# Kernel tuning notes

Measured on AMD Instinct MI355X. Metric: run time of the kernel, lower is better.

Reference implementation:

```python
import jax, jax.numpy as jnp
import numpy as np

B, T, S, C, F = 32, 50, 2048, 8, 32  # batch, time, spatial steps, in-channels, filters
K, STRIDE = 2, 2
DN = ('NWC', 'WIO', 'NWC')


def hard_sigmoid(x):
    # TF-Keras hard_sigmoid: clip(0.2*x + 0.5, 0, 1)
    return jnp.clip(0.2 * x + 0.5, 0.0, 1.0)


def setup_inputs() -> dict:
    key = jax.random.key(0)
    ks = jax.random.split(key, 5)
    x = jax.random.normal(ks[0], (B, T, S, C), jnp.float32)
    kernel = jax.random.normal(ks[1], (K, C, 4 * F), jnp.float32) * 0.05
    rec_kernel = jax.random.normal(ks[2], (K, F, 4 * F), jnp.float32) * 0.05
    bias = jnp.zeros((4 * F,), jnp.float32)
    dense_w = jax.random.normal(ks[3], ((S // STRIDE) * F, 1), jnp.float32) * 0.02
    dense_b = jnp.zeros((1,), jnp.float32)
    return dict(x=x, kernel=kernel, rec_kernel=rec_kernel, bias=bias,
                dense_w=dense_w, dense_b=dense_b)


def reference(x, kernel, rec_kernel, bias, dense_w, dense_b):
    b, t, s, c = x.shape
    f = rec_kernel.shape[1]
    # Input convolution for all timesteps at once (stride 2, SAME padding)
    xc = jax.lax.conv_general_dilated(x.reshape(b * t, s, c), kernel,
                                      (STRIDE,), 'SAME', dimension_numbers=DN)
    xc = xc + bias
    sh = xc.shape[1]  # ceil(s / stride)
    xc = xc.reshape(b, t, sh, 4 * f).transpose(1, 0, 2, 3)  # time-major for scan

    def step(carry, xt):
        h, cst = carry
        hc = jax.lax.conv_general_dilated(h, rec_kernel, (1,), 'SAME',
                                          dimension_numbers=DN)
        z = xt + hc
        zi, zf, zc, zo = jnp.split(z, 4, axis=-1)
        i = hard_sigmoid(zi)
        fg = hard_sigmoid(zf)
        cst = fg * cst + i * jnp.tanh(zc)
        o = hard_sigmoid(zo)
        h = o * jnp.tanh(cst)
        return (h, cst), None

    h0 = jnp.zeros((b, sh, f), x.dtype)
    (h, _), _ = jax.lax.scan(step, (h0, h0), xc)
    # Flatten + Dense(1)
    return h.reshape(b, -1) @ dense_w + dense_b
```

## Files before the change

kernel.cpp:

```cpp
#include <hip/hip_runtime.h>


#define TT 50
#define LTILE 64
#define ROWS 129
#define HSTR 40

typedef __attribute__((ext_vector_type(8))) short short8;
typedef __attribute__((ext_vector_type(4))) float floatx4;

__device__ __forceinline__ unsigned short f2b_rne(float f) {
  union { float f; unsigned u; } v; v.f = f;
  unsigned r = v.u + 0x7FFFu + ((v.u >> 16) & 1u);
  return (unsigned short)(r >> 16);
}
__device__ __forceinline__ unsigned short f2b_trunc(float f) {
  union { float f; unsigned u; } v; v.f = f;
  return (unsigned short)(v.u >> 16);
}
__device__ __forceinline__ float hsig(float x) {
  return __builtin_amdgcn_fmed3f(__builtin_fmaf(0.2f, x, 0.5f), 0.0f, 1.0f);
}
__device__ __forceinline__ float ftanh(float x) {
  float e = __expf(2.0f * x);
  return 1.0f - 2.0f * __builtin_amdgcn_rcpf(e + 1.0f);
}

__global__ __launch_bounds__(256, 2)
void convlstm_scan(const float* __restrict__ xs,
                   const float* __restrict__ ks,
                   const float* __restrict__ rks,
                   const float* __restrict__ bs,
                   const float* __restrict__ dws,
                   float* __restrict__ acc_out) {
  __shared__ short hbH[2][ROWS * HSTR];

  const int tid  = threadIdx.x;
  const int b    = blockIdx.x >> 4;
  const int j0   = (blockIdx.x & 15) * LTILE;
  const int wave = tid >> 6;
  const int lane = tid & 63;
  const int q    = lane >> 4;
  const int f0   = lane & 15;

  for (int e = tid; e < ROWS * HSTR; e += 256)
    ((int*)hbH)[e] = 0;

  short8 Bwh0[8], Bwh1[8], Bxw[8];
#pragma unroll
  for (int n = 0; n < 8; ++n) {
    const int oc = (n >> 1) * 32 + 2 * f0 + (n & 1);
    short8 th;
#pragma unroll
    for (int j = 0; j < 8; ++j)
      th[j] = (short)f2b_rne(rks[(q * 8 + j) * 128 + oc]);
    Bwh0[n] = th;
#pragma unroll
    for (int j = 0; j < 8; ++j)
      th[j] = (short)f2b_rne(rks[(32 + q * 8 + j) * 128 + oc]);
    Bwh1[n] = th;
    short8 tx = {0, 0, 0, 0, 0, 0, 0, 0};
    if (q < 2) {
#pragma unroll
      for (int j = 0; j < 8; ++j)
        tx[j] = (short)f2b_rne(ks[(q * 8 + j) * 128 + oc]);
    } else if (q == 2) {
      tx[0] = (short)f2b_rne(bs[oc]);
    }
    Bxw[n] = tx;
  }

  short8 axc = {0, 0, 0, 0, 0, 0, 0, 0};
  if (q == 2) axc[0] = (short)0x3F80;

  const floatx4 zero4 = {0.0f, 0.0f, 0.0f, 0.0f};

  float cst[2][8];
#pragma unroll
  for (int s = 0; s < 2; ++s)
#pragma unroll
    for (int i = 0; i < 8; ++i) cst[s][i] = 0.0f;

  floatx4 px0[2], px1[2];
#pragma unroll
  for (int s = 0; s < 2; ++s) {
    const int jr = (wave + 4 * s) * 16 + f0;
    const int jm = min(j0 + jr, 1023);
    const float* xp = xs + (size_t)b * TT * (2048 * 8) +
                      (size_t)(2 * jm + (q & 1)) * 8;
    px0[s] = *(const floatx4*)xp;
    px1[s] = *(const floatx4*)(xp + 4);
  }

  const int maxrows = 1024 - j0;
  float part = 0.0f;
  __syncthreads();

  for (int t = 0; t < TT; ++t) {
    const short* curH = hbH[t & 1];
    short* nxtH = hbH[(t & 1) ^ 1];
    int rows = LTILE + (TT - 1) - t;
    if (rows > maxrows) rows = maxrows;
    const int nmt = (rows + 15) >> 4;
    const int act1 = (wave + 4) < nmt;
    const int last = (t == TT - 1);
    const int tn = last ? t : t + 1;
    const float* xnext = xs + ((size_t)(b * TT + tn)) * (2048 * 8);

    short8 a0h[2], a1h[2];
#pragma unroll
    for (int s = 0; s < 2; ++s) {
      const int jr = (wave + 4 * s) * 16 + f0;
      a0h[s] = *(const short8*)&curH[jr * HSTR + q * 8];
      a1h[s] = *(const short8*)&curH[(jr + 1) * HSTR + q * 8];
    }

    short8 ax[2];
#pragma unroll
    for (int s = 0; s < 2; ++s) {
      ax[s] = axc;
      if (q < 2) {
        floatx4 x0 = px0[s], x1 = px1[s];
#pragma unroll
        for (int jj = 0; jj < 4; ++jj) ax[s][jj] = (short)f2b_trunc(x0[jj]);
#pragma unroll
        for (int jj = 0; jj < 4; ++jj) ax[s][4 + jj] = (short)f2b_trunc(x1[jj]);
      }
    }

#pragma unroll
    for (int s = 0; s < 2; ++s) {
      const int jr = (wave + 4 * s) * 16 + f0;
      const int jm = min(j0 + jr, 1023);
      const float* xp = xnext + (size_t)(2 * jm + (q & 1)) * 8;
      px0[s] = *(const floatx4*)xp;
      px1[s] = *(const floatx4*)(xp + 4);
    }

#pragma unroll
    for (int s = 0; s < 2; ++s) {
      if (s == 1 && !act1) continue;
      const int m = wave + 4 * s;

      floatx4 acc[8];
#pragma unroll
      for (int n = 0; n < 8; ++n)
        acc[n] = __builtin_amdgcn_mfma_f32_16x16x32_bf16(ax[s], Bxw[n], zero4, 0, 0, 0);
#pragma unroll
      for (int n = 0; n < 8; ++n)
        acc[n] = __builtin_amdgcn_mfma_f32_16x16x32_bf16(a0h[s], Bwh0[n], acc[n], 0, 0, 0);
#pragma unroll
      for (int n = 0; n < 8; ++n)
        acc[n] = __builtin_amdgcn_mfma_f32_16x16x32_bf16(a1h[s], Bwh1[n], acc[n], 0, 0, 0);

      const int jw = m * 16 + q * 4;
#pragma unroll
      for (int r = 0; r < 4; ++r) {
        float hv2[2];
#pragma unroll
        for (int p = 0; p < 2; ++p) {
          float zi = acc[0 + p][r], zf = acc[2 + p][r];
          float zc = acc[4 + p][r], zo = acc[6 + p][r];
          float ig = hsig(zi), fg = hsig(zf), og = hsig(zo);
          float cs = cst[s][p * 4 + r];
          float cn = __builtin_fmaf(fg, cs, ig * ftanh(zc));
          cst[s][p * 4 + r] = cn;
          hv2[p] = og * ftanh(cn);
        }
        if (!last) {
          unsigned pk = (unsigned)f2b_rne(hv2[0]) |
                        ((unsigned)f2b_rne(hv2[1]) << 16);
          *(unsigned*)&nxtH[(jw + r) * HSTR + 2 * f0] = pk;
        } else {
          const int di = (j0 + jw + r) * 32 + 2 * f0;
          part = __builtin_fmaf(hv2[0], dws[di],
                 __builtin_fmaf(hv2[1], dws[di + 1], part));
        }
      }
    }
    __syncthreads();
  }

#pragma unroll
  for (int off = 32; off > 0; off >>= 1) part += __shfl_down(part, off);
  if (lane == 0) atomicAdd(&acc_out[b], part);
}

__global__ void init_acc(float* ws) {
  if (threadIdx.x < 32) ws[threadIdx.x] = 0.0f;
}

__global__ void finalize(const float* __restrict__ ws,
                         const float* __restrict__ db,
                         float* __restrict__ out) {
  int i = threadIdx.x;
  if (i < 32) out[i] = ws[i] + db[0];
}

extern "C" void kernel_launch(void* const* d_in, const int* in_sizes, int n_in,
                              void* d_out, int out_size, void* d_ws, size_t ws_size,
                              hipStream_t stream) {
  const float* x  = (const float*)d_in[0];
  const float* k  = (const float*)d_in[1];
  const float* rk = (const float*)d_in[2];
  const float* bi = (const float*)d_in[3];
  const float* dw = (const float*)d_in[4];
  const float* db = (const float*)d_in[5];
  float* ws = (float*)d_ws;
  float* out = (float*)d_out;

  hipLaunchKernelGGL(init_acc, dim3(1), dim3(64), 0, stream, ws);
  hipLaunchKernelGGL(convlstm_scan, dim3(512), dim3(256), 0, stream,
                     x, k, rk, bi, dw, ws);
  hipLaunchKernelGGL(finalize, dim3(1), dim3(64), 0, stream, ws, db, out);
}
```

Measured before the change: 240.6 us.

## Split gate output columns across two wave halves with 512-thread blocks

```diff
diff --git a/kernel.cpp b/kernel.cpp
--- a/kernel.cpp
+++ b/kernel.cpp
@@ -26,7 +26,7 @@
   return 1.0f - 2.0f * __builtin_amdgcn_rcpf(e + 1.0f);
 }
 
-__global__ __launch_bounds__(256, 2)
+__global__ __launch_bounds__(512, 4)
 void convlstm_scan(const float* __restrict__ xs,
                    const float* __restrict__ ks,
                    const float* __restrict__ rks,
@@ -39,26 +39,28 @@
   const int b    = blockIdx.x >> 4;
   const int j0   = (blockIdx.x & 15) * LTILE;
   const int wave = tid >> 6;
+  const int mw   = wave & 3;
+  const int p    = wave >> 2;
   const int lane = tid & 63;
   const int q    = lane >> 4;
   const int f0   = lane & 15;
 
-  for (int e = tid; e < ROWS * HSTR; e += 256)
+  for (int e = tid; e < ROWS * HSTR; e += 512)
     ((int*)hbH)[e] = 0;
 
-  short8 Bwh0[8], Bwh1[8], Bxw[8];
-#pragma unroll
-  for (int n = 0; n < 8; ++n) {
-    const int oc = (n >> 1) * 32 + 2 * f0 + (n & 1);
+  short8 Bwh0[4], Bwh1[4], Bxw[4];
+#pragma unroll
+  for (int g = 0; g < 4; ++g) {
+    const int oc = g * 32 + 2 * f0 + p;
     short8 th;
 #pragma unroll
     for (int j = 0; j < 8; ++j)
       th[j] = (short)f2b_rne(rks[(q * 8 + j) * 128 + oc]);
-    Bwh0[n] = th;
+    Bwh0[g] = th;
 #pragma unroll
     for (int j = 0; j < 8; ++j)
       th[j] = (short)f2b_rne(rks[(32 + q * 8 + j) * 128 + oc]);
-    Bwh1[n] = th;
+    Bwh1[g] = th;
     short8 tx = {0, 0, 0, 0, 0, 0, 0, 0};
     if (q < 2) {
 #pragma unroll
@@ -67,7 +69,7 @@
     } else if (q == 2) {
       tx[0] = (short)f2b_rne(bs[oc]);
     }
-    Bxw[n] = tx;
+    Bxw[g] = tx;
   }
 
   short8 axc = {0, 0, 0, 0, 0, 0, 0, 0};
@@ -75,16 +77,16 @@
 
   const floatx4 zero4 = {0.0f, 0.0f, 0.0f, 0.0f};
 
-  float cst[2][8];
+  float cst[2][4];
 #pragma unroll
   for (int s = 0; s < 2; ++s)
 #pragma unroll
-    for (int i = 0; i < 8; ++i) cst[s][i] = 0.0f;
+    for (int i = 0; i < 4; ++i) cst[s][i] = 0.0f;
 
   floatx4 px0[2], px1[2];
 #pragma unroll
   for (int s = 0; s < 2; ++s) {
-    const int jr = (wave + 4 * s) * 16 + f0;
+    const int jr = (mw + 4 * s) * 16 + f0;
     const int jm = min(j0 + jr, 1023);
     const float* xp = xs + (size_t)b * TT * (2048 * 8) +
                       (size_t)(2 * jm + (q & 1)) * 8;
@@ -102,7 +104,7 @@
     int rows = LTILE + (TT - 1) - t;
     if (rows > maxrows) rows = maxrows;
     const int nmt = (rows + 15) >> 4;
-    const int act1 = (wave + 4) < nmt;
+    const int act1 = (mw + 4) < nmt;
     const int last = (t == TT - 1);
     const int tn = last ? t : t + 1;
     const float* xnext = xs + ((size_t)(b * TT + tn)) * (2048 * 8);
@@ -110,7 +112,7 @@
     short8 a0h[2], a1h[2];
 #pragma unroll
     for (int s = 0; s < 2; ++s) {
-      const int jr = (wave + 4 * s) * 16 + f0;
+      const int jr = (mw + 4 * s) * 16 + f0;
       a0h[s] = *(const short8*)&curH[jr * HSTR + q * 8];
       a1h[s] = *(const short8*)&curH[(jr + 1) * HSTR + q * 8];
     }
@@ -130,7 +132,7 @@
 
 #pragma unroll
     for (int s = 0; s < 2; ++s) {
-      const int jr = (wave + 4 * s) * 16 + f0;
+      const int jr = (mw + 4 * s) * 16 + f0;
       const int jm = min(j0 + jr, 1023);
       const float* xp = xnext + (size_t)(2 * jm + (q & 1)) * 8;
       px0[s] = *(const floatx4*)xp;
@@ -140,41 +142,34 @@
 #pragma unroll
     for (int s = 0; s < 2; ++s) {
       if (s == 1 && !act1) continue;
-      const int m = wave + 4 * s;
-
-      floatx4 acc[8];
-#pragma unroll
-      for (int n = 0; n < 8; ++n)
-        acc[n] = __builtin_amdgcn_mfma_f32_16x16x32_bf16(ax[s], Bxw[n], zero4, 0, 0, 0);
-#pragma unroll
-      for (int n = 0; n < 8; ++n)
-        acc[n] = __builtin_amdgcn_mfma_f32_16x16x32_bf16(a0h[s], Bwh0[n], acc[n], 0, 0, 0);
-#pragma unroll
-      for (int n = 0; n < 8; ++n)
-        acc[n] = __builtin_amdgcn_mfma_f32_16x16x32_bf16(a1h[s], Bwh1[n], acc[n], 0, 0, 0);
+      const int m = mw + 4 * s;
+
+      floatx4 acc[4];
+#pragma unroll
+      for (int g = 0; g < 4; ++g)
+        acc[g] = __builtin_amdgcn_mfma_f32_16x16x32_bf16(ax[s], Bxw[g], zero4, 0, 0, 0);
+#pragma unroll
+      for (int g = 0; g < 4; ++g)
+        acc[g] = __builtin_amdgcn_mfma_f32_16x16x32_bf16(a0h[s], Bwh0[g], acc[g], 0, 0, 0);
+#pragma unroll
+      for (int g = 0; g < 4; ++g)
+        acc[g] = __builtin_amdgcn_mfma_f32_16x16x32_bf16(a1h[s], Bwh1[g], acc[g], 0, 0, 0);
 
       const int jw = m * 16 + q * 4;
 #pragma unroll
       for (int r = 0; r < 4; ++r) {
-        float hv2[2];
-#pragma unroll
-        for (int p = 0; p < 2; ++p) {
-          float zi = acc[0 + p][r], zf = acc[2 + p][r];
-          float zc = acc[4 + p][r], zo = acc[6 + p][r];
-          float ig = hsig(zi), fg = hsig(zf), og = hsig(zo);
-          float cs = cst[s][p * 4 + r];
-          float cn = __builtin_fmaf(fg, cs, ig * ftanh(zc));
-          cst[s][p * 4 + r] = cn;
-          hv2[p] = og * ftanh(cn);
-        }
+        float zi = acc[0][r], zf = acc[1][r];
+        float zc = acc[2][r], zo = acc[3][r];
+        float ig = hsig(zi), fg = hsig(zf), og = hsig(zo);
+        float cs = cst[s][r];
+        float cn = __builtin_fmaf(fg, cs, ig * ftanh(zc));
+        cst[s][r] = cn;
+        float hv = og * ftanh(cn);
         if (!last) {
-          unsigned pk = (unsigned)f2b_rne(hv2[0]) |
-                        ((unsigned)f2b_rne(hv2[1]) << 16);
-          *(unsigned*)&nxtH[(jw + r) * HSTR + 2 * f0] = pk;
+          nxtH[(jw + r) * HSTR + 2 * f0 + p] = (short)f2b_rne(hv);
         } else {
-          const int di = (j0 + jw + r) * 32 + 2 * f0;
-          part = __builtin_fmaf(hv2[0], dws[di],
-                 __builtin_fmaf(hv2[1], dws[di + 1], part));
+          const int di = (j0 + jw + r) * 32 + 2 * f0 + p;
+          part = __builtin_fmaf(hv, dws[di], part);
         }
       }
     }
@@ -210,7 +205,7 @@
   float* out = (float*)d_out;
 
   hipLaunchKernelGGL(init_acc, dim3(1), dim3(64), 0, stream, ws);
-  hipLaunchKernelGGL(convlstm_scan, dim3(512), dim3(256), 0, stream,
+  hipLaunchKernelGGL(convlstm_scan, dim3(512), dim3(512), 0, stream,
                      x, k, rk, bi, dw, ws);
   hipLaunchKernelGGL(finalize, dim3(1), dim3(64), 0, stream, ws, db, out);
 }
```

Result: slower. 257.8 us (+7.1%).
